# Optimization experiments

Hardware: AMD Instinct MI355X
Metric: run time of the kernel (lower is better)

Reference implementation:

```python
import jax, jax.numpy as jnp
import numpy as np

DX = 0.04                      # params.dx
D0 = 0.0005 / DX ** 2          # params.D_eff[0] = 0.3125
BC00 = 1.0                     # BC[0, 0]


def _mlp(x, W1, b1, W2, b2, W3, b3, W4, b4):
    # create_mlp([1,15,15,15,1], Tanh(), Sigmoid())
    h = jnp.tanh(x @ W1 + b1)
    h = jnp.tanh(h @ W2 + b2)
    h = jnp.tanh(h @ W3 + b3)
    return jax.nn.sigmoid(h @ W4 + b4)


def setup_inputs() -> dict:
    key = jax.random.key(0)
    ks = jax.random.split(key, 6)
    N, T = 65536, 33
    c0 = jax.random.uniform(ks[0], (N,), jnp.float32)
    t = jnp.arange(T, dtype=jnp.float32) * 5.0  # params.dt = 5

    def lin(k, fan_in, fan_out):
        bnd = 1.0 / np.sqrt(fan_in)
        kw, kb = jax.random.split(k)
        W = jax.random.uniform(kw, (fan_in, fan_out), jnp.float32, -bnd, bnd)
        b = jax.random.uniform(kb, (fan_out,), jnp.float32, -bnd, bnd)
        return W, b

    W1, b1 = lin(ks[1], 1, 15)
    W2, b2 = lin(ks[2], 15, 15)
    W3, b3 = lin(ks[3], 15, 15)
    W4, b4 = lin(ks[4], 15, 1)
    p_exp = jnp.array([1.0], jnp.float32)
    return dict(c0=c0, t=t, W1=W1, b1=b1, W2=W2, b2=b2,
                W3=W3, b3=b3, W4=W4, b4=b4, p_exp=p_exp)


def reference(c0, t, W1, b1, W2, b2, W3, b3, W4, b4, p_exp):
    scale = 10.0 ** p_exp[0]

    def flux(c):
        # scaled_ret_inv(c).squeeze(-1): [N]
        ret = _mlp((c * scale)[:, None], W1, b1, W2, b2, W3, b3, W4, b4)[:, 0]
        # left fluxes (stencil = [-1, 1])
        left_bound = (D0 * ret[0] * (BC00 - c[0]))[None]
        left_nb = D0 * ret[1:] * (c[:-1] - c[1:])
        left = jnp.concatenate([left_bound, left_nb])
        # right fluxes with Cauchy-type right BC
        right_bc = D0 * DX * (c[-2] - c[-1])
        right_bound = (D0 * ret[-1] * (right_bc - c[-1]))[None]
        right_nb = D0 * ret[:-1] * (c[1:] - c[:-1])
        right = jnp.concatenate([right_nb, right_bound])
        return left + right

    def step(c, dt):
        # classic RK4 step of dc/dt = flux(c)
        k1 = flux(c)
        k2 = flux(c + 0.5 * dt * k1)
        k3 = flux(c + 0.5 * dt * k2)
        k4 = flux(c + dt * k3)
        c_new = c + (dt / 6.0) * (k1 + 2.0 * k2 + 2.0 * k3 + k4)
        return c_new, c_new

    dts = t[1:] - t[:-1]
    _, ys = jax.lax.scan(step, c0, dts)
    return jnp.concatenate([c0[None], ys], axis=0)  # [T, N]
```

## Files before the change

kernel.cpp:

```cpp
#include <hip/hip_runtime.h>
#include <math.h>


constexpr int TPB     = 512;
constexpr int S_FUSE  = 32;
constexpr int HALO    = 4 * S_FUSE;
constexpr int B_INNER = TPB - 2 * HALO;

constexpr int   NTAB   = 5633;
constexpr float VSLOPE = 88.72283911167299f;
constexpr float VOFF   = 2816.0f;
constexpr float HSTEP  = 0.0078125f;
constexpr int   NSEG   = NTAB - 1;

constexpr int F_SCALE = 4 * NSEG;
constexpr int F_A0    = 4 * NSEG + 1;
constexpr int F_TOT   = 4 * NSEG + 1 + 32;
constexpr int F4_TOT  = (F_TOT + 3) / 4;

__device__ __forceinline__ float fast_tanh(float x) {
    float e = __expf(2.0f * x);
    return 1.0f - 2.0f * __builtin_amdgcn_rcpf(1.0f + e);
}

__global__ __launch_bounds__(256)
void build_tab_kernel(const float* __restrict__ W1, const float* __restrict__ b1,
                      const float* __restrict__ W2, const float* __restrict__ b2,
                      const float* __restrict__ W3, const float* __restrict__ b3,
                      const float* __restrict__ W4, const float* __restrict__ b4,
                      const float* __restrict__ p_exp, const float* __restrict__ t,
                      int nsteps, float* __restrict__ wsf)
{
    const int i = blockIdx.x * blockDim.x + threadIdx.x;
    if (i > NTAB) {
        const int s = i - NTAB - 1;
        if (s < nsteps && s < 32)
            wsf[F_A0 + s] = (t[s + 1] - t[s]) * 0.3125f;
        return;
    }
    if (i == NTAB) {
        wsf[F_SCALE] = powf(10.0f, p_exp[0]);
        return;
    }
    const float u  = -22.0f + (float)i * HSTEP;
    const float y  = sinhf(u);
    const float yd = coshf(u);

    float h[15], hd[15], g[15], gd[15];
#pragma unroll
    for (int j = 0; j < 15; ++j) {
        float a  = fmaf(y, W1[j], b1[j]);
        float ad = yd * W1[j];
        float th = fast_tanh(a);
        h[j]  = th;
        hd[j] = (1.0f - th * th) * ad;
    }
#pragma unroll
    for (int j = 0; j < 15; ++j) {
        float a = b2[j], ad = 0.0f;
#pragma unroll
        for (int k = 0; k < 15; ++k) {
            a  = fmaf(h[k],  W2[k * 15 + j], a);
            ad = fmaf(hd[k], W2[k * 15 + j], ad);
        }
        float th = fast_tanh(a);
        g[j]  = th;
        gd[j] = (1.0f - th * th) * ad;
    }
#pragma unroll
    for (int j = 0; j < 15; ++j) {
        float a = b3[j], ad = 0.0f;
#pragma unroll
        for (int k = 0; k < 15; ++k) {
            a  = fmaf(g[k],  W3[k * 15 + j], a);
            ad = fmaf(gd[k], W3[k * 15 + j], ad);
        }
        float th = fast_tanh(a);
        h[j]  = th;
        hd[j] = (1.0f - th * th) * ad;
    }
    float o = b4[0], od = 0.0f;
#pragma unroll
    for (int k = 0; k < 15; ++k) {
        o  = fmaf(h[k],  W4[k], o);
        od = fmaf(hd[k], W4[k], od);
    }
    const float s = __builtin_amdgcn_rcpf(1.0f + __expf(-o));
    const float d = s * (1.0f - s) * od;
    if (i < NSEG) {
        wsf[4 * i]     = s;
        wsf[4 * i + 1] = d;
    }
    if (i > 0) {
        wsf[4 * (i - 1) + 2] = s;
        wsf[4 * (i - 1) + 3] = d;
    }
}

__device__ __forceinline__ float ret_tab(float c, float scale,
                                         const float4* __restrict__ tab4)
{
    const float y  = c * scale;
    const float ay = fabsf(y);
    const float w  = ay + __builtin_amdgcn_sqrtf(fmaf(ay, ay, 1.0f));
    const float m  = copysignf(VSLOPE, y);
    float v = fmaf(__builtin_amdgcn_logf(w), m, VOFF);
    v = fminf(fmaxf(v, 0.0f), (float)(NSEG - 1) + 0.999f);
    const int   i   = (int)v;
    const float tau = v - (float)i;

    const float4 AB = tab4[i];
    const float t2 = tau * tau;
    const float t3 = t2 * tau;
    return AB.x * (2.0f * t3 - 3.0f * t2 + 1.0f)
         + AB.z * (3.0f * t2 - 2.0f * t3)
         + HSTEP * (AB.y * (t3 - 2.0f * t2 + tau) + AB.w * (t3 - t2));
}

__device__ __forceinline__ float flux_cell(float ret, float c, float cl, float cr,
                                           int g, int N)
{
    if (g == 0)
        return ret * ((1.0f - c) + (cr - c));
    if (g == N - 1) {
        float rbc = 0.0125f * (cl - c);
        return ret * ((cl - c) + (rbc - c));
    }
    return ret * (cl + cr - 2.0f * c);
}

#define STAGE_BARRIER()                                            \
    do {                                                           \
        __builtin_amdgcn_sched_barrier(0);                         \
        asm volatile("s_waitcnt lgkmcnt(0)\n\ts_barrier" ::: "memory"); \
        __builtin_amdgcn_sched_barrier(0);                         \
    } while (0)

__global__ __launch_bounds__(TPB)
void rk4_steps_kernel(const float* __restrict__ src,
                      float* __restrict__ out,
                      const float* __restrict__ wsf,
                      int N, int s0, int nsub)
{
    __shared__ float tlds[F4_TOT * 4];
    __shared__ float la[TPB + 2];
    __shared__ float lb[TPB + 2];

    const int tid = threadIdx.x;

    {
        const float4* __restrict__ s4 = (const float4*)wsf;
        float4* d4 = (float4*)tlds;
        for (int i = tid; i < F4_TOT; i += TPB) d4[i] = s4[i];
    }

    const int g  = blockIdx.x * B_INNER - HALO + tid;
    const int gi = min(max(g, 0), N - 1);

    float c = src[gi];

    const bool valid = (tid >= HALO) && (tid < HALO + B_INNER) && (g < N);

    if (s0 == 0 && valid) out[g] = c;

    __syncthreads();
    const float4* __restrict__ tab4 = (const float4*)tlds;
    const float scale = tlds[F_SCALE];

    for (int s = 0; s < nsub; ++s) {
        const float A = tlds[F_A0 + s];

        float ret1 = ret_tab(c, scale, tab4);
        la[tid + 1] = c;
        STAGE_BARRIER();
        float cl = la[tid], cr = la[tid + 2];
        float k1 = flux_cell(ret1, c, cl, cr, g, N);
        float c2 = fmaf(0.5f * A, k1, c);

        float ret2 = ret_tab(c2, scale, tab4);
        lb[tid + 1] = c2;
        STAGE_BARRIER();
        cl = lb[tid]; cr = lb[tid + 2];
        float k2 = flux_cell(ret2, c2, cl, cr, g, N);
        float c3 = fmaf(0.5f * A, k2, c);

        float ret3 = ret_tab(c3, scale, tab4);
        la[tid + 1] = c3;
        STAGE_BARRIER();
        cl = la[tid]; cr = la[tid + 2];
        float k3 = flux_cell(ret3, c3, cl, cr, g, N);
        float c4 = fmaf(A, k3, c);

        float ret4 = ret_tab(c4, scale, tab4);
        lb[tid + 1] = c4;
        STAGE_BARRIER();
        cl = lb[tid]; cr = lb[tid + 2];
        float k4 = flux_cell(ret4, c4, cl, cr, g, N);

        c = fmaf(A * (1.0f / 6.0f), k1 + 2.0f * (k2 + k3) + k4, c);

        if (valid)
            out[(size_t)(s0 + s + 1) * N + g] = c;
    }
}

extern "C" void kernel_launch(void* const* d_in, const int* in_sizes, int n_in,
                              void* d_out, int out_size, void* d_ws, size_t ws_size,
                              hipStream_t stream)
{
    const float* c0    = (const float*)d_in[0];
    const float* t     = (const float*)d_in[1];
    const float* W1    = (const float*)d_in[2];
    const float* b1    = (const float*)d_in[3];
    const float* W2    = (const float*)d_in[4];
    const float* b2    = (const float*)d_in[5];
    const float* W3    = (const float*)d_in[6];
    const float* b3    = (const float*)d_in[7];
    const float* W4    = (const float*)d_in[8];
    const float* b4    = (const float*)d_in[9];
    const float* p_exp = (const float*)d_in[10];

    float* out = (float*)d_out;
    float* wsf = (float*)d_ws;

    const int N      = in_sizes[0];
    const int nsteps = in_sizes[1] - 1;

    const int tgrid = (NTAB + 1 + 32 + 255) / 256;
    hipLaunchKernelGGL(build_tab_kernel, dim3(tgrid), dim3(256), 0, stream,
                       W1, b1, W2, b2, W3, b3, W4, b4, p_exp, t, nsteps, wsf);

    const int grid = (N + B_INNER - 1) / B_INNER;

    for (int s0 = 0; s0 < nsteps; s0 += S_FUSE) {
        const int nsub = min(S_FUSE, nsteps - s0);
        const float* src = (s0 == 0) ? c0 : out + (size_t)s0 * N;
        hipLaunchKernelGGL(rk4_steps_kernel, dim3(grid), dim3(TPB), 0, stream,
                           src, out, wsf, N, s0, nsub);
    }
}
```

Baseline: 46.39 us.

## Process two cells per thread with 256-thread blocks over 512-cell windows

New measurement: 56.69 us. 22.2% more time.

```diff
diff --git a/kernel.cpp b/kernel.cpp
--- a/kernel.cpp
+++ b/kernel.cpp
@@ -2,10 +2,11 @@
 #include <math.h>
 
 
-constexpr int TPB     = 512;
+constexpr int TPB     = 256;
+constexpr int WIN     = 512;
 constexpr int S_FUSE  = 32;
 constexpr int HALO    = 4 * S_FUSE;
-constexpr int B_INNER = TPB - 2 * HALO;
+constexpr int B_INNER = WIN - 2 * HALO;
 
 constexpr int   NTAB   = 5633;
 constexpr float VSLOPE = 88.72283911167299f;
@@ -117,18 +118,6 @@
          + HSTEP * (AB.y * (t3 - 2.0f * t2 + tau) + AB.w * (t3 - t2));
 }
 
-__device__ __forceinline__ float flux_cell(float ret, float c, float cl, float cr,
-                                           int g, int N)
-{
-    if (g == 0)
-        return ret * ((1.0f - c) + (cr - c));
-    if (g == N - 1) {
-        float rbc = 0.0125f * (cl - c);
-        return ret * ((cl - c) + (rbc - c));
-    }
-    return ret * (cl + cr - 2.0f * c);
-}
-
 #define STAGE_BARRIER()                                            \
     do {                                                           \
         __builtin_amdgcn_sched_barrier(0);                         \
@@ -143,8 +132,8 @@
                       int N, int s0, int nsub)
 {
     __shared__ float tlds[F4_TOT * 4];
-    __shared__ float la[TPB + 2];
-    __shared__ float lb[TPB + 2];
+    __shared__ float la[WIN];
+    __shared__ float lb[WIN];
 
     const int tid = threadIdx.x;
 
@@ -154,14 +143,22 @@
         for (int i = tid; i < F4_TOT; i += TPB) d4[i] = s4[i];
     }
 
-    const int g  = blockIdx.x * B_INNER - HALO + tid;
-    const int gi = min(max(g, 0), N - 1);
-
-    float c = src[gi];
-
-    const bool valid = (tid >= HALO) && (tid < HALO + B_INNER) && (g < N);
-
-    if (s0 == 0 && valid) out[g] = c;
+    const int base = blockIdx.x * B_INNER - HALO;
+    const int w0   = 2 * tid;
+    const int g0   = base + w0;
+    const int g1   = g0 + 1;
+
+    float cx = src[min(max(g0, 0), N - 1)];
+    float cy = src[min(max(g1, 0), N - 1)];
+
+    const int iu = max(w0 - 1, 0);
+    const int id = min(w0 + 2, WIN - 1);
+
+    const bool valid = (w0 >= HALO) && (w0 < HALO + B_INNER);
+
+    if (s0 == 0 && valid && (unsigned)g0 < (unsigned)N - 1) {
+        *(float2*)(out + g0) = make_float2(cx, cy);
+    }
 
     __syncthreads();
     const float4* __restrict__ tab4 = (const float4*)tlds;
@@ -170,37 +167,63 @@
     for (int s = 0; s < nsub; ++s) {
         const float A = tlds[F_A0 + s];
 
-        float ret1 = ret_tab(c, scale, tab4);
-        la[tid + 1] = c;
-        STAGE_BARRIER();
-        float cl = la[tid], cr = la[tid + 2];
-        float k1 = flux_cell(ret1, c, cl, cr, g, N);
-        float c2 = fmaf(0.5f * A, k1, c);
-
-        float ret2 = ret_tab(c2, scale, tab4);
-        lb[tid + 1] = c2;
-        STAGE_BARRIER();
-        cl = lb[tid]; cr = lb[tid + 2];
-        float k2 = flux_cell(ret2, c2, cl, cr, g, N);
-        float c3 = fmaf(0.5f * A, k2, c);
-
-        float ret3 = ret_tab(c3, scale, tab4);
-        la[tid + 1] = c3;
-        STAGE_BARRIER();
-        cl = la[tid]; cr = la[tid + 2];
-        float k3 = flux_cell(ret3, c3, cl, cr, g, N);
-        float c4 = fmaf(A, k3, c);
-
-        float ret4 = ret_tab(c4, scale, tab4);
-        lb[tid + 1] = c4;
-        STAGE_BARRIER();
-        cl = lb[tid]; cr = lb[tid + 2];
-        float k4 = flux_cell(ret4, c4, cl, cr, g, N);
-
-        c = fmaf(A * (1.0f / 6.0f), k1 + 2.0f * (k2 + k3) + k4, c);
-
-        if (valid)
-            out[(size_t)(s0 + s + 1) * N + g] = c;
+        float r1x = ret_tab(cx, scale, tab4);
+        float r1y = ret_tab(cy, scale, tab4);
+        *(float2*)(la + w0) = make_float2(cx, cy);
+        STAGE_BARRIER();
+        float lft = la[iu], rgt = la[id];
+        float k1x, k1y;
+        if (g0 == 0)          k1x = r1x * ((1.0f - cx) + (cy - cx));
+        else                  k1x = r1x * (lft + cy - 2.0f * cx);
+        if (g1 == N - 1)      k1y = r1y * ((cx - cy) + (0.0125f * (cx - cy) - cy));
+        else                  k1y = r1y * (cx + rgt - 2.0f * cy);
+        float c2x = fmaf(0.5f * A, k1x, cx);
+        float c2y = fmaf(0.5f * A, k1y, cy);
+
+        float r2x = ret_tab(c2x, scale, tab4);
+        float r2y = ret_tab(c2y, scale, tab4);
+        *(float2*)(lb + w0) = make_float2(c2x, c2y);
+        STAGE_BARRIER();
+        lft = lb[iu]; rgt = lb[id];
+        float k2x, k2y;
+        if (g0 == 0)          k2x = r2x * ((1.0f - c2x) + (c2y - c2x));
+        else                  k2x = r2x * (lft + c2y - 2.0f * c2x);
+        if (g1 == N - 1)      k2y = r2y * ((c2x - c2y) + (0.0125f * (c2x - c2y) - c2y));
+        else                  k2y = r2y * (c2x + rgt - 2.0f * c2y);
+        float c3x = fmaf(0.5f * A, k2x, cx);
+        float c3y = fmaf(0.5f * A, k2y, cy);
+
+        float r3x = ret_tab(c3x, scale, tab4);
+        float r3y = ret_tab(c3y, scale, tab4);
+        *(float2*)(la + w0) = make_float2(c3x, c3y);
+        STAGE_BARRIER();
+        lft = la[iu]; rgt = la[id];
+        float k3x, k3y;
+        if (g0 == 0)          k3x = r3x * ((1.0f - c3x) + (c3y - c3x));
+        else                  k3x = r3x * (lft + c3y - 2.0f * c3x);
+        if (g1 == N - 1)      k3y = r3y * ((c3x - c3y) + (0.0125f * (c3x - c3y) - c3y));
+        else                  k3y = r3y * (c3x + rgt - 2.0f * c3y);
+        float c4x = fmaf(A, k3x, cx);
+        float c4y = fmaf(A, k3y, cy);
+
+        float r4x = ret_tab(c4x, scale, tab4);
+        float r4y = ret_tab(c4y, scale, tab4);
+        *(float2*)(lb + w0) = make_float2(c4x, c4y);
+        STAGE_BARRIER();
+        lft = lb[iu]; rgt = lb[id];
+        float k4x, k4y;
+        if (g0 == 0)          k4x = r4x * ((1.0f - c4x) + (c4y - c4x));
+        else                  k4x = r4x * (lft + c4y - 2.0f * c4x);
+        if (g1 == N - 1)      k4y = r4y * ((c4x - c4y) + (0.0125f * (c4x - c4y) - c4y));
+        else                  k4y = r4y * (c4x + rgt - 2.0f * c4y);
+
+        cx = fmaf(A * (1.0f / 6.0f), k1x + 2.0f * (k2x + k3x) + k4x, cx);
+        cy = fmaf(A * (1.0f / 6.0f), k1y + 2.0f * (k2y + k3y) + k4y, cy);
+
+        if (valid && (unsigned)g0 < (unsigned)N - 1) {
+            float* row = out + (size_t)(s0 + s + 1) * N;
+            *(float2*)(row + g0) = make_float2(cx, cy);
+        }
     }
 }
 
```
